# Kernel tuning notes

Measured on AMD Instinct MI355X. Metric: run time of the kernel, lower is better.

## Reference

```python
import jax, jax.numpy as jnp
import numpy as np

N_EVENTS = 16384
B = 4
H = W = 64
KH = KW = 3
P = KH * KW
D = 256  # input_size == hidden_size


def setup_inputs() -> dict:
    rng = np.random.default_rng(0)
    # events sorted by batch, time = arange (sorted within batch)
    batch_id = np.sort(rng.integers(0, B, N_EVENTS))
    hh = rng.integers(KH - 1, H - KH + 1, N_EVENTS)  # interior pixels -> exactly P patches each
    ww = rng.integers(KW - 1, W - KW + 1, N_EVENTS)
    time = np.arange(N_EVENTS)
    # scatter each event to its P=kh*kw overlapping patches (stride 1)
    Hp, Wp = H - KH + 1, W - KW + 1
    ki = np.arange(KH)[:, None]
    kj = np.arange(KW)[None, :]
    pos = (ki * KW + kj).reshape(1, P)                       # [1, P]
    pl = hh[:, None] - ki.reshape(1, -1).repeat(KW, 1).reshape(1, P) if False else None
    ki_f = np.repeat(np.arange(KH), KW)                       # [P]
    kj_f = np.tile(np.arange(KW), KH)                         # [P]
    patch_row = hh[:, None] - ki_f[None, :]                   # [N, P]
    patch_col = ww[:, None] - kj_f[None, :]
    patch_lin = (batch_id[:, None] * (Hp * Wp) + patch_row * Wp + patch_col).reshape(-1)
    pos_flat = np.broadcast_to((ki_f * KW + kj_f)[None, :], (N_EVENTS, P)).reshape(-1)
    orig_flat = np.repeat(np.arange(N_EVENTS), P)
    t_flat = np.repeat(time, P)
    order = np.lexsort((t_flat, patch_lin))                   # group by patch, time-ordered within
    patch_sorted = patch_lin[order]
    orig_event_idx = orig_flat[order].astype(np.int32)
    pos_id = pos_flat[order].astype(np.int32)
    seg_start = np.concatenate([[True], patch_sorted[1:] != patch_sorted[:-1]])

    key = jax.random.key(0)
    ks = jax.random.split(key, 8)
    std = np.sqrt(2.0 / (D + D)).astype(np.float32)
    lin = 1.0 / np.sqrt(D).astype(np.float32)
    return {
        "events": jax.random.normal(ks[0], (N_EVENTS, D), jnp.float32),
        "scatter_w": jax.random.normal(ks[1], (P, D, D), jnp.float32) * std,
        "gather_w": jax.random.normal(ks[2], (P, D, D), jnp.float32) * std,
        "q_w": jax.random.normal(ks[3], (D, D), jnp.float32) * lin,
        "v_w": jax.random.normal(ks[4], (D, D), jnp.float32) * lin,
        "g_w": jax.random.normal(ks[5], (D, D), jnp.float32) * lin,
        "o_w": jax.random.normal(ks[6], (D, D), jnp.float32) * lin,
        "ln_gamma": jnp.ones((D,), jnp.float32),
        "ln_beta": jnp.zeros((D,), jnp.float32),
        "orig_event_idx": jnp.asarray(orig_event_idx),
        "pos_id": jnp.asarray(pos_id),
        "seg_start": jnp.asarray(seg_start),
    }


def _pos_proj(x, weights, pos_id):
    # per-patch-position linear: out[n] = weights[pos_id[n]] @ x[n]
    # disjoint masks partition rows, so masked GEMMs sum exactly (mirrors torch loop)
    out = jnp.zeros((x.shape[0], weights.shape[1]), x.dtype)
    for i in range(weights.shape[0]):
        m = (pos_id == i)[:, None]
        out = out + jnp.where(m, x @ weights[i].T, 0.0)
    return out


def _gated_scan(g, v, seg_start):
    # h_t = g_t * h_{t-1} + (1 - g_t) * v_t, reset at segment starts
    a = jnp.where(seg_start[:, None], 0.0, g)
    b = (1.0 - g) * v
    def comb(c1, c2):
        a1, b1 = c1
        a2, b2 = c2
        return (a1 * a2, a2 * b1 + b2)
    _, h = jax.lax.associative_scan(comb, (a, b), axis=0)
    return h


def reference(events, scatter_w, gather_w, q_w, v_w, g_w, o_w, ln_gamma, ln_beta,
              orig_event_idx, pos_id, seg_start):
    x = events[orig_event_idx]                     # [M, D] scatter events -> patch copies
    y = _pos_proj(x, scatter_w, pos_id)            # indexed conv-like projection
    q = y @ q_w.T
    v = y @ v_w.T
    g = jax.nn.sigmoid(y @ g_w.T)
    h = _gated_scan(g, v, seg_start)               # ragged gated linear scan
    o = (q * h) @ o_w.T
    z = _pos_proj(o, gather_w, pos_id)             # indexed gather projection
    out = jnp.zeros_like(events).at[orig_event_idx].add(z)  # gather back (sum over P copies)
    out = out + events                             # residual (input_size == hidden_size)
    mu = jnp.mean(out, axis=-1, keepdims=True)
    var = jnp.mean(jnp.square(out - mu), axis=-1, keepdims=True)
    out = (out - mu) * jax.lax.rsqrt(var + 1e-5) * ln_gamma + ln_beta
    return out
```

## Files before the change

### kernel.cpp

```cpp
#include <hip/hip_runtime.h>

typedef __bf16 bf16x8 __attribute__((ext_vector_type(8)));
typedef float f32x4 __attribute__((ext_vector_type(4)));

#define NEV 16384
#define MTOT 147456
#define LDQ 2304
#define LDX 6912

__device__ __forceinline__ unsigned short f2bf(float f) {
  unsigned x = __float_as_uint(f);
  x += 0x7FFFu + ((x >> 16) & 1u);
  return (unsigned short)(x >> 16);
}
__device__ __forceinline__ float bf2f(unsigned short u) {
  return __uint_as_float(((unsigned)u) << 16);
}
__device__ __forceinline__ void load_lds16(const void* g, void* l) {
  __builtin_amdgcn_global_load_lds(
      (const __attribute__((address_space(1))) unsigned int*)g,
      (__attribute__((address_space(3))) unsigned int*)l, 16, 0, 0);
}

__global__ void k_cast4(const float* __restrict__ in, unsigned short* __restrict__ out, int n4) {
  int i = blockIdx.x * blockDim.x + threadIdx.x;
  if (i >= n4) return;
  float4 v = reinterpret_cast<const float4*>(in)[i];
  ushort4 o;
  o.x = f2bf(v.x); o.y = f2bf(v.y); o.z = f2bf(v.z); o.w = f2bf(v.w);
  reinterpret_cast<ushort4*>(out)[i] = o;
}

__global__ void k_cast3(const float* __restrict__ q, const float* __restrict__ v,
                        const float* __restrict__ g, unsigned short* __restrict__ out) {
  int which = blockIdx.y;
  const float* src = (which == 0) ? q : (which == 1) ? v : g;
  int i = blockIdx.x * blockDim.x + threadIdx.x;
  if (i >= 16384) return;
  float4 val = reinterpret_cast<const float4*>(src)[i];
  ushort4 o;
  o.x = f2bf(val.x); o.y = f2bf(val.y); o.z = f2bf(val.z); o.w = f2bf(val.w);
  reinterpret_cast<ushort4*>(out + (long)which * 65536)[i] = o;
}

__global__ __launch_bounds__(256) void k_transpose_t(const float* __restrict__ in,
                                                     unsigned short* __restrict__ out) {
  __shared__ float s[32][33];
  const int b = blockIdx.z;
  const int r0 = blockIdx.x * 32, c0 = blockIdx.y * 32;
  const int tx = threadIdx.x & 31, ty = threadIdx.x >> 5;
  const float* src = in + (long)b * 65536;
  unsigned short* dst = out + (long)b * 65536;
#pragma unroll
  for (int cc = 0; cc < 4; ++cc)
    s[ty + cc * 8][tx] = src[(c0 + ty + cc * 8) * 256 + r0 + tx];
  __syncthreads();
#pragma unroll
  for (int cc = 0; cc < 4; ++cc)
    dst[(long)(r0 + ty + cc * 8) * 256 + c0 + tx] = f2bf(s[tx][ty + cc * 8]);
}

__global__ void k_detect(const unsigned int* __restrict__ seg, int* mode) {
  __shared__ int fFloat, fGt1;
  if (threadIdx.x == 0) { fFloat = 0; fGt1 = 0; }
  __syncthreads();
  int lf = 0, lg = 0;
  for (int i = threadIdx.x; i < 1024; i += 256) {
    unsigned v = seg[i];
    if (v == 0x3F800000u) lf = 1;
    else if (v > 1u) lg = 1;
  }
  if (lf) atomicOr(&fFloat, 1);
  if (lg) atomicOr(&fGt1, 1);
  __syncthreads();
  if (threadIdx.x == 0) *mode = fFloat ? 2 : (fGt1 ? 1 : 0);
}

__device__ __forceinline__ bool is_start(const void* seg, int mode, int i) {
  if (mode == 1) return ((const unsigned char*)seg)[i] != 0;
  if (mode == 2) return ((const float*)seg)[i] != 0.0f;
  return ((const int*)seg)[i] != 0;
}

__global__ __launch_bounds__(256) void k_count(const void* __restrict__ seg,
                                               const int* __restrict__ modep,
                                               int* __restrict__ blockCounts) {
  __shared__ int wc[4];
  const int md = *modep;
  const int i = blockIdx.x * 256 + threadIdx.x;
  const bool f = is_start(seg, md, i);
  unsigned long long m = __ballot(f);
  const int lane = threadIdx.x & 63, wid = threadIdx.x >> 6;
  if (lane == 0) wc[wid] = __popcll(m);
  __syncthreads();
  if (threadIdx.x == 0) blockCounts[blockIdx.x] = wc[0] + wc[1] + wc[2] + wc[3];
}

__global__ __launch_bounds__(256) void k_emit(const void* __restrict__ seg,
                                              const int* __restrict__ modep,
                                              const int* __restrict__ blockCounts,
                                              int* __restrict__ starts, int* __restrict__ nsegp) {
  __shared__ int sh[12];
  const int md = *modep;
  const int bid = blockIdx.x, tid = threadIdx.x;
  const int lane = tid & 63, wid = tid >> 6;
  int part = 0;
  for (int j = tid; j < bid; j += 256) part += blockCounts[j];
  for (int o = 32; o; o >>= 1) part += __shfl_xor(part, o, 64);
  if (lane == 0) sh[wid] = part;
  if (bid == 0) {
    int tot = 0;
    for (int j = tid; j < 576; j += 256) tot += blockCounts[j];
    for (int o = 32; o; o >>= 1) tot += __shfl_xor(tot, o, 64);
    if (lane == 0) sh[8 + wid] = tot;
  }
  const int i = bid * 256 + tid;
  const bool f = is_start(seg, md, i);
  unsigned long long m = __ballot(f);
  if (lane == 0) sh[4 + wid] = __popcll(m);
  __syncthreads();
  const int base = sh[0] + sh[1] + sh[2] + sh[3];
  int wpre = 0;
#pragma unroll
  for (int w2 = 0; w2 < 4; ++w2) if (w2 < wid) wpre += sh[4 + w2];
  if (bid == 0 && tid == 0) *nsegp = sh[8] + sh[9] + sh[10] + sh[11];
  if (f) {
    const int lanePre = __popcll(m & ((1ull << lane) - 1));
    starts[base + wpre + lanePre] = i;
  }
}

template<bool F32OUT>
__device__ __forceinline__ void gemm_tile(
    const unsigned short* __restrict__ A, const unsigned short* __restrict__ B,
    void* __restrict__ Cv, int r0, int c0, int K, int lda, int ldb, int ldc,
    unsigned short* As, unsigned short* Bs) {
  const int tid = threadIdx.x, lane = tid & 63, wid = tid >> 6;
  const int wr = (wid >> 1) * 64, wc = (wid & 1) * 64;
  const int la = lane & 15, lb2 = lane >> 4;
  const int arow = tid >> 2;
  const int cs = ((tid & 3) ^ ((arow >> 1) & 3)) * 8;
  const int nk = K >> 5;
  f32x4 acc[4][4];
#pragma unroll
  for (int i = 0; i < 4; ++i)
#pragma unroll
    for (int j = 0; j < 4; ++j) acc[i][j] = (f32x4)0.0f;

  const unsigned short* ga0 = A + (long)(r0 + arow) * lda + cs;
  const unsigned short* gb0 = B + (long)(c0 + arow) * ldb + cs;

  load_lds16(ga0, &As[tid * 8]);
  load_lds16(ga0 + (long)64 * lda, &As[2048 + tid * 8]);
  load_lds16(gb0, &Bs[tid * 8]);
  load_lds16(gb0 + (long)64 * ldb, &Bs[2048 + tid * 8]);
  __syncthreads();

  for (int k = 0; k < nk; ++k) {
    if (k + 1 < nk) {
      const int nb = ((k + 1) & 1) * 4096;
      const unsigned short* ga = ga0 + (k + 1) * 32;
      const unsigned short* gb = gb0 + (k + 1) * 32;
      load_lds16(ga, &As[nb + tid * 8]);
      load_lds16(ga + (long)64 * lda, &As[nb + 2048 + tid * 8]);
      load_lds16(gb, &Bs[nb + tid * 8]);
      load_lds16(gb + (long)64 * ldb, &Bs[nb + 2048 + tid * 8]);
    }
    const int cb = (k & 1) * 4096;
    bf16x8 af[4], bv[4];
#pragma unroll
    for (int i = 0; i < 4; ++i) {
      const int ra = wr + i * 16 + la;
      const int rb = wc + i * 16 + la;
      af[i] = *reinterpret_cast<const bf16x8*>(&As[cb + ra * 32 + ((lb2 ^ ((ra >> 1) & 3)) * 8)]);
      bv[i] = *reinterpret_cast<const bf16x8*>(&Bs[cb + rb * 32 + ((lb2 ^ ((rb >> 1) & 3)) * 8)]);
    }
#pragma unroll
    for (int i = 0; i < 4; ++i)
#pragma unroll
      for (int j = 0; j < 4; ++j)
        acc[i][j] = __builtin_amdgcn_mfma_f32_16x16x32_bf16(af[i], bv[j], acc[i][j], 0, 0, 0);
    __syncthreads();
  }
#pragma unroll
  for (int i = 0; i < 4; ++i)
#pragma unroll
    for (int j = 0; j < 4; ++j)
#pragma unroll
      for (int r = 0; r < 4; ++r) {
        const int row = r0 + wr + i * 16 + lb2 * 4 + r;
        const int col = c0 + wc + j * 16 + la;
        if (F32OUT) ((float*)Cv)[(long)row * ldc + col] = acc[i][j][r];
        else ((unsigned short*)Cv)[(long)row * ldc + col] = f2bf(acc[i][j][r]);
      }
}

__global__ __launch_bounds__(256) void k_wgemm(
    const unsigned short* __restrict__ qvgw, const unsigned short* __restrict__ wt,
    const unsigned short* __restrict__ gaw, const unsigned short* __restrict__ owt,
    unsigned short* __restrict__ ABig, unsigned short* __restrict__ Bo2) {
  __shared__ __align__(16) unsigned short As[8192];
  __shared__ __align__(16) unsigned short Bs[8192];
  const int b = blockIdx.z;
  const unsigned short *A, *B;
  unsigned short* C;
  int ldc;
  if (b < 27) {
    A = qvgw + (long)(b / 9) * 65536;
    B = wt + (long)(b % 9) * 65536;
    C = ABig + (long)b * 65536; ldc = 256;
  } else {
    A = gaw + (long)(b - 27) * 65536;
    B = owt;
    C = Bo2 + (b - 27) * 256; ldc = LDQ;
  }
  gemm_tile<false>(A, B, C, blockIdx.x * 128, blockIdx.y * 128, 256, 256, 256, ldc, As, Bs);
}

__global__ __launch_bounds__(256) void k_qvg3(
    const unsigned short* __restrict__ ev, const unsigned short* __restrict__ ABig,
    unsigned short* __restrict__ X) {
  __shared__ __align__(16) unsigned short As[8192];
  __shared__ __align__(16) unsigned short Bs[3][4096];
  const int p = blockIdx.z;
  const int r0 = blockIdx.x * 128, c0 = blockIdx.y * 64;
  const int tid = threadIdx.x, lane = tid & 63, wid = tid >> 6;
  const int wr2 = (wid >> 1) * 64, wc2 = (wid & 1) * 32;
  const int la = lane & 15, lb2 = lane >> 4;
  f32x4 acc[3][4][2];
#pragma unroll
  for (int w = 0; w < 3; ++w)
#pragma unroll
    for (int i = 0; i < 4; ++i)
#pragma unroll
      for (int j = 0; j < 2; ++j) acc[w][i][j] = (f32x4)0.0f;

  for (int k0 = 0; k0 < 256; k0 += 64) {
#pragma unroll
    for (int q = 0; q < 4; ++q) {
      const int g = q * 256 + tid;
      const int row = g >> 3, c = g & 7;
      load_lds16(ev + (long)(r0 + row) * 256 + k0 + ((c ^ (row & 7)) * 8), &As[g * 8]);
    }
#pragma unroll
    for (int w = 0; w < 3; ++w) {
      const unsigned short* Bw = ABig + (long)(w * 9 + p) * 65536;
#pragma unroll
      for (int q = 0; q < 2; ++q) {
        const int g = q * 256 + tid;
        const int row = g >> 3, c = g & 7;
        load_lds16(Bw + (long)(c0 + row) * 256 + k0 + ((c ^ (row & 7)) * 8), &Bs[w][g * 8]);
      }
    }
    __syncthreads();
#pragma unroll
    for (int kk = 0; kk < 2; ++kk) {
      bf16x8 af[4], bv[3][2];
#pragma unroll
      for (int i = 0; i < 4; ++i) {
        const int ra = wr2 + i * 16 + la;
        const int slot = (kk * 4 + lb2) ^ (ra & 7);
        af[i] = *reinterpret_cast<const bf16x8*>(&As[ra * 64 + slot * 8]);
      }
#pragma unroll
      for (int w = 0; w < 3; ++w)
#pragma unroll
        for (int j = 0; j < 2; ++j) {
          const int rb = wc2 + j * 16 + la;
          const int slot = (kk * 4 + lb2) ^ (rb & 7);
          bv[w][j] = *reinterpret_cast<const bf16x8*>(&Bs[w][rb * 64 + slot * 8]);
        }
#pragma unroll
      for (int w = 0; w < 3; ++w)
#pragma unroll
        for (int i = 0; i < 4; ++i)
#pragma unroll
          for (int j = 0; j < 2; ++j)
            acc[w][i][j] = __builtin_amdgcn_mfma_f32_16x16x32_bf16(af[i], bv[w][j], acc[w][i][j], 0, 0, 0);
    }
    __syncthreads();
  }
#pragma unroll
  for (int w = 0; w < 3; ++w) {
    unsigned short* Xw = X + p * 768 + w * 256;
#pragma unroll
    for (int i = 0; i < 4; ++i)
#pragma unroll
      for (int j = 0; j < 2; ++j)
#pragma unroll
        for (int r = 0; r < 4; ++r) {
          const int row = r0 + wr2 + i * 16 + lb2 * 4 + r;
          const int col = c0 + wc2 + j * 16 + la;
          Xw[(long)row * LDX + col] = f2bf(acc[w][i][j][r]);
        }
  }
}

__global__ __launch_bounds__(256) void k_scan(
    unsigned short* __restrict__ X,
    const int* __restrict__ starts, const int* __restrict__ cntp, const int* __restrict__ modep,
    const void* __restrict__ seg, const int* __restrict__ pos_id, const int* __restrict__ oidx) {
  const int lane = threadIdx.x & 63;
  const int w = blockIdx.x * 4 + (threadIdx.x >> 6);
  const int nW = gridDim.x * 4;
  const int nseg = *cntp;
  const int md = *modep;
  for (int s = w; s < nseg; s += nW) {
    int t = starts[s];
    int p = pos_id[t], e = oidx[t];
    long base = (long)e * LDX + p * 768 + lane * 4;
    ushort4 ql = *(const ushort4*)(X + base);
    ushort4 vl = *(const ushort4*)(X + base + 256);
    ushort4 gl = *(const ushort4*)(X + base + 512);
    bool cont = (t + 1 < MTOT) && !is_start(seg, md, t + 1);
    float h0 = 0.f, h1 = 0.f, h2 = 0.f, h3 = 0.f;
    for (;;) {
      ushort4 qn, vn, gn;
      long nbase = 0;
      bool cont2 = false;
      if (cont) {
        int pn = pos_id[t + 1], en = oidx[t + 1];
        nbase = (long)en * LDX + pn * 768 + lane * 4;
        qn = *(const ushort4*)(X + nbase);
        vn = *(const ushort4*)(X + nbase + 256);
        gn = *(const ushort4*)(X + nbase + 512);
        cont2 = (t + 2 < MTOT) && !is_start(seg, md, t + 2);
      }
      float g0 = 1.f / (1.f + __expf(-bf2f(gl.x)));
      float g1 = 1.f / (1.f + __expf(-bf2f(gl.y)));
      float g2 = 1.f / (1.f + __expf(-bf2f(gl.z)));
      float g3 = 1.f / (1.f + __expf(-bf2f(gl.w)));
      h0 = g0 * h0 + (1.f - g0) * bf2f(vl.x);
      h1 = g1 * h1 + (1.f - g1) * bf2f(vl.y);
      h2 = g2 * h2 + (1.f - g2) * bf2f(vl.z);
      h3 = g3 * h3 + (1.f - g3) * bf2f(vl.w);
      ushort4 o;
      o.x = f2bf(bf2f(ql.x) * h0);
      o.y = f2bf(bf2f(ql.y) * h1);
      o.z = f2bf(bf2f(ql.z) * h2);
      o.w = f2bf(bf2f(ql.w) * h3);
      *(ushort4*)(X + base + 256) = o;
      if (!cont) break;
      ++t;
      base = nbase; ql = qn; vl = vn; gl = gn; cont = cont2;
    }
  }
}

__global__ __launch_bounds__(256) void k_p5(
    const unsigned short* __restrict__ X, const unsigned short* __restrict__ Bo2,
    const float* __restrict__ ev, float* __restrict__ S) {
  __shared__ __align__(16) unsigned short As[4096];
  __shared__ __align__(16) unsigned short Bs[4096];
  const int r0 = blockIdx.x * 128, c0 = blockIdx.y * 128;
  const int tid = threadIdx.x, lane = tid & 63, wid = tid >> 6;
  const int wr = (wid >> 1) * 64, wc = (wid & 1) * 64;
  const int la = lane & 15, lb2 = lane >> 4;
  const int arow = tid >> 2;
  const int cs = ((tid & 3) ^ ((arow >> 1) & 3)) * 8;
  f32x4 acc[4][4];
#pragma unroll
  for (int i = 0; i < 4; ++i)
#pragma unroll
    for (int j = 0; j < 4; ++j) acc[i][j] = (f32x4)0.0f;

  for (int kc = 0; kc < 72; ++kc) {
    const int p = kc >> 3, nn = (kc & 7) * 32;
    const unsigned short* ga = X + (long)(r0 + arow) * LDX + p * 768 + 256 + nn + cs;
    const unsigned short* gb = Bo2 + (long)(c0 + arow) * LDQ + p * 256 + nn + cs;
    load_lds16(ga, &As[tid * 8]);
    load_lds16(ga + (long)64 * LDX, &As[2048 + tid * 8]);
    load_lds16(gb, &Bs[tid * 8]);
    load_lds16(gb + (long)64 * LDQ, &Bs[2048 + tid * 8]);
    __syncthreads();
    bf16x8 af[4], bv[4];
#pragma unroll
    for (int i = 0; i < 4; ++i) {
      const int ra = wr + i * 16 + la;
      const int rb = wc + i * 16 + la;
      af[i] = *reinterpret_cast<const bf16x8*>(&As[ra * 32 + ((lb2 ^ ((ra >> 1) & 3)) * 8)]);
      bv[i] = *reinterpret_cast<const bf16x8*>(&Bs[rb * 32 + ((lb2 ^ ((rb >> 1) & 3)) * 8)]);
    }
#pragma unroll
    for (int i = 0; i < 4; ++i)
#pragma unroll
      for (int j = 0; j < 4; ++j)
        acc[i][j] = __builtin_amdgcn_mfma_f32_16x16x32_bf16(af[i], bv[j], acc[i][j], 0, 0, 0);
    __syncthreads();
  }
#pragma unroll
  for (int i = 0; i < 4; ++i)
#pragma unroll
    for (int j = 0; j < 4; ++j)
#pragma unroll
      for (int r = 0; r < 4; ++r) {
        const int row = r0 + wr + i * 16 + lb2 * 4 + r;
        const int col = c0 + wc + j * 16 + la;
        S[(long)row * 256 + col] = acc[i][j][r] + ev[(long)row * 256 + col];
      }
}

__global__ __launch_bounds__(256) void k_ln(float* __restrict__ S,
                                            const float* __restrict__ gamma, const float* __restrict__ beta) {
  int row = blockIdx.x * 4 + (threadIdx.x >> 6);
  int lane = threadIdx.x & 63;
  long base = (long)row * 256 + lane * 4;
  float4 s4 = *reinterpret_cast<const float4*>(S + base);
  float v0 = s4.x, v1 = s4.y, v2 = s4.z, v3 = s4.w;
  float s = v0 + v1 + v2 + v3;
  float ss = v0 * v0 + v1 * v1 + v2 * v2 + v3 * v3;
  for (int o = 32; o; o >>= 1) { s += __shfl_xor(s, o, 64); ss += __shfl_xor(ss, o, 64); }
  float mu = s * (1.0f / 256.0f);
  float var = ss * (1.0f / 256.0f) - mu * mu;
  float rs = rsqrtf(fmaxf(var, 0.0f) + 1e-5f);
  float4 g4 = *reinterpret_cast<const float4*>(gamma + lane * 4);
  float4 b4 = *reinterpret_cast<const float4*>(beta + lane * 4);
  float4 o4;
  o4.x = (v0 - mu) * rs * g4.x + b4.x;
  o4.y = (v1 - mu) * rs * g4.y + b4.y;
  o4.z = (v2 - mu) * rs * g4.z + b4.z;
  o4.w = (v3 - mu) * rs * g4.w + b4.w;
  *reinterpret_cast<float4*>(S + base) = o4;
}

extern "C" void kernel_launch(void* const* d_in, const int* in_sizes, int n_in,
                              void* d_out, int out_size, void* d_ws, size_t ws_size,
                              hipStream_t stream) {
  const float* events    = (const float*)d_in[0];
  const float* scatter_w = (const float*)d_in[1];
  const float* gather_w  = (const float*)d_in[2];
  const float* q_w       = (const float*)d_in[3];
  const float* v_w       = (const float*)d_in[4];
  const float* g_w       = (const float*)d_in[5];
  const float* o_w       = (const float*)d_in[6];
  const float* ln_gamma  = (const float*)d_in[7];
  const float* ln_beta   = (const float*)d_in[8];
  const int*   oidx      = (const int*)d_in[9];
  const int*   pos_id    = (const int*)d_in[10];
  const void*  seg       = d_in[11];
  float* out = (float*)d_out;

  char* base = (char*)d_ws;
  int* counter = (int*)base;
  int* mode    = (int*)(base + 4);
  int* blockCounts = (int*)(base + 64);
  int* starts  = (int*)(base + 4096);
  unsigned short* ev_bf  = (unsigned short*)(base + 598016);
  unsigned short* wt     = (unsigned short*)(base + 8986624);
  unsigned short* qvgw   = (unsigned short*)(base + 10166272);
  unsigned short* owt    = (unsigned short*)(base + 10559488);
  unsigned short* gaw_bf = (unsigned short*)(base + 10690560);
  unsigned short* ABig   = (unsigned short*)(base + 11870208);
  unsigned short* Bo2    = (unsigned short*)(base + 15409152);
  unsigned short* X      = (unsigned short*)(base + 16588800);

  k_detect<<<1, 256, 0, stream>>>((const unsigned int*)seg, mode);

  k_cast4<<<4096, 256, 0, stream>>>(events, ev_bf, 1048576);
  k_cast3<<<dim3(64, 3), 256, 0, stream>>>(q_w, v_w, g_w, qvgw);
  k_cast4<<<576, 256, 0, stream>>>(gather_w, gaw_bf, 147456);
  k_transpose_t<<<dim3(8, 8, 9), 256, 0, stream>>>(scatter_w, wt);
  k_transpose_t<<<dim3(8, 8, 1), 256, 0, stream>>>(o_w, owt);

  k_wgemm<<<dim3(2, 2, 36), 256, 0, stream>>>(qvgw, wt, gaw_bf, owt, ABig, Bo2);

  k_qvg3<<<dim3(128, 4, 9), 256, 0, stream>>>(ev_bf, ABig, X);

  k_count<<<576, 256, 0, stream>>>(seg, mode, blockCounts);
  k_emit<<<576, 256, 0, stream>>>(seg, mode, blockCounts, starts, counter);
  k_scan<<<2048, 256, 0, stream>>>(X, starts, counter, mode, seg, pos_id, oidx);

  k_p5<<<dim3(128, 2), 256, 0, stream>>>(X, Bo2, events, out);
  k_ln<<<4096, 256, 0, stream>>>(out, ln_gamma, ln_beta);
}
```

Measured before the change: 228.3 us.

## Fuse cast kernels, merge transposes, and fold LayerNorm into final GEMM

```diff
diff --git a/kernel.cpp b/kernel.cpp
--- a/kernel.cpp
+++ b/kernel.cpp
@@ -22,35 +22,40 @@
       (__attribute__((address_space(3))) unsigned int*)l, 16, 0, 0);
 }
 
-__global__ void k_cast4(const float* __restrict__ in, unsigned short* __restrict__ out, int n4) {
+__global__ void k_prep(const float* __restrict__ events, const float* __restrict__ q,
+                       const float* __restrict__ v, const float* __restrict__ g,
+                       const float* __restrict__ gaw,
+                       unsigned short* __restrict__ ev_bf, unsigned short* __restrict__ qvgw,
+                       unsigned short* __restrict__ gaw_bf) {
   int i = blockIdx.x * blockDim.x + threadIdx.x;
-  if (i >= n4) return;
-  float4 v = reinterpret_cast<const float4*>(in)[i];
-  ushort4 o;
-  o.x = f2bf(v.x); o.y = f2bf(v.y); o.z = f2bf(v.z); o.w = f2bf(v.w);
-  reinterpret_cast<ushort4*>(out)[i] = o;
-}
-
-__global__ void k_cast3(const float* __restrict__ q, const float* __restrict__ v,
-                        const float* __restrict__ g, unsigned short* __restrict__ out) {
-  int which = blockIdx.y;
-  const float* src = (which == 0) ? q : (which == 1) ? v : g;
-  int i = blockIdx.x * blockDim.x + threadIdx.x;
-  if (i >= 16384) return;
-  float4 val = reinterpret_cast<const float4*>(src)[i];
+  const float* src;
+  unsigned short* dst;
+  int off;
+  if (i < 1048576) { src = events; dst = ev_bf; off = i; }
+  else if (i < 1097728) {
+    int j = i - 1048576;
+    int w = j >> 14;
+    src = (w == 0) ? q : (w == 1) ? v : g;
+    dst = qvgw + (long)w * 65536;
+    off = j & 16383;
+  } else if (i < 1245184) { src = gaw; dst = gaw_bf; off = i - 1097728; }
+  else return;
+  float4 val = reinterpret_cast<const float4*>(src)[off];
   ushort4 o;
   o.x = f2bf(val.x); o.y = f2bf(val.y); o.z = f2bf(val.z); o.w = f2bf(val.w);
-  reinterpret_cast<ushort4*>(out + (long)which * 65536)[i] = o;
-}
-
-__global__ __launch_bounds__(256) void k_transpose_t(const float* __restrict__ in,
-                                                     unsigned short* __restrict__ out) {
+  reinterpret_cast<ushort4*>(dst)[off] = o;
+}
+
+__global__ __launch_bounds__(256) void k_transpose_t(const float* __restrict__ sw,
+                                                     const float* __restrict__ ow,
+                                                     unsigned short* __restrict__ wt,
+                                                     unsigned short* __restrict__ owt) {
   __shared__ float s[32][33];
-  const int b = blockIdx.z;
+  const int z = blockIdx.z;
+  const float* src = (z < 9) ? sw + (long)z * 65536 : ow;
+  unsigned short* dst = (z < 9) ? wt + (long)z * 65536 : owt;
   const int r0 = blockIdx.x * 32, c0 = blockIdx.y * 32;
   const int tx = threadIdx.x & 31, ty = threadIdx.x >> 5;
-  const float* src = in + (long)b * 65536;
-  unsigned short* dst = out + (long)b * 65536;
 #pragma unroll
   for (int cc = 0; cc < 4; ++cc)
     s[ty + cc * 8][tx] = src[(c0 + ty + cc * 8) * 256 + r0 + tx];
@@ -130,10 +135,9 @@
   }
 }
 
-template<bool F32OUT>
 __device__ __forceinline__ void gemm_tile(
     const unsigned short* __restrict__ A, const unsigned short* __restrict__ B,
-    void* __restrict__ Cv, int r0, int c0, int K, int lda, int ldb, int ldc,
+    unsigned short* __restrict__ C, int r0, int c0, int K, int lda, int ldb, int ldc,
     unsigned short* As, unsigned short* Bs) {
   const int tid = threadIdx.x, lane = tid & 63, wid = tid >> 6;
   const int wr = (wid >> 1) * 64, wc = (wid & 1) * 64;
@@ -190,8 +194,7 @@
       for (int r = 0; r < 4; ++r) {
         const int row = r0 + wr + i * 16 + lb2 * 4 + r;
         const int col = c0 + wc + j * 16 + la;
-        if (F32OUT) ((float*)Cv)[(long)row * ldc + col] = acc[i][j][r];
-        else ((unsigned short*)Cv)[(long)row * ldc + col] = f2bf(acc[i][j][r]);
+        C[(long)row * ldc + col] = f2bf(acc[i][j][r]);
       }
 }
 
@@ -214,7 +217,7 @@
     B = owt;
     C = Bo2 + (b - 27) * 256; ldc = LDQ;
   }
-  gemm_tile<false>(A, B, C, blockIdx.x * 128, blockIdx.y * 128, 256, 256, 256, ldc, As, Bs);
+  gemm_tile(A, B, C, blockIdx.x * 128, blockIdx.y * 128, 256, 256, 256, ldc, As, Bs);
 }
 
 __global__ __launch_bounds__(256) void k_qvg3(
@@ -347,17 +350,21 @@
   }
 }
 
-__global__ __launch_bounds__(256) void k_p5(
+__global__ __launch_bounds__(512) void k_p5ln(
     const unsigned short* __restrict__ X, const unsigned short* __restrict__ Bo2,
-    const float* __restrict__ ev, float* __restrict__ S) {
+    const float* __restrict__ ev, const float* __restrict__ gamma,
+    const float* __restrict__ beta, float* __restrict__ out) {
   __shared__ __align__(16) unsigned short As[4096];
-  __shared__ __align__(16) unsigned short Bs[4096];
-  const int r0 = blockIdx.x * 128, c0 = blockIdx.y * 128;
+  __shared__ __align__(16) unsigned short Bs[8192];
+  __shared__ float rsum[128], rsumsq[128];
+  const int r0 = blockIdx.x * 128;
   const int tid = threadIdx.x, lane = tid & 63, wid = tid >> 6;
-  const int wr = (wid >> 1) * 64, wc = (wid & 1) * 64;
+  const int wr = (wid >> 2) * 64, wc = (wid & 3) * 64;
   const int la = lane & 15, lb2 = lane >> 4;
-  const int arow = tid >> 2;
-  const int cs = ((tid & 3) ^ ((arow >> 1) & 3)) * 8;
+  if (tid < 128) { rsum[tid] = 0.0f; rsumsq[tid] = 0.0f; }
+
+  const int arowA = tid >> 2;
+  const int csA = ((tid & 3) ^ ((arowA >> 1) & 3)) * 8;
   f32x4 acc[4][4];
 #pragma unroll
   for (int i = 0; i < 4; ++i)
@@ -366,12 +373,14 @@
 
   for (int kc = 0; kc < 72; ++kc) {
     const int p = kc >> 3, nn = (kc & 7) * 32;
-    const unsigned short* ga = X + (long)(r0 + arow) * LDX + p * 768 + 256 + nn + cs;
-    const unsigned short* gb = Bo2 + (long)(c0 + arow) * LDQ + p * 256 + nn + cs;
-    load_lds16(ga, &As[tid * 8]);
-    load_lds16(ga + (long)64 * LDX, &As[2048 + tid * 8]);
-    load_lds16(gb, &Bs[tid * 8]);
-    load_lds16(gb + (long)64 * LDQ, &Bs[2048 + tid * 8]);
+    load_lds16(X + (long)(r0 + arowA) * LDX + p * 768 + 256 + nn + csA, &As[tid * 8]);
+#pragma unroll
+    for (int q = 0; q < 2; ++q) {
+      const int g = q * 512 + tid;
+      const int rowB = g >> 2;
+      const int cB = ((g & 3) ^ ((rowB >> 1) & 3)) * 8;
+      load_lds16(Bo2 + (long)rowB * LDQ + p * 256 + nn + cB, &Bs[g * 8]);
+    }
     __syncthreads();
     bf16x8 af[4], bv[4];
 #pragma unroll
@@ -388,39 +397,40 @@
         acc[i][j] = __builtin_amdgcn_mfma_f32_16x16x32_bf16(af[i], bv[j], acc[i][j], 0, 0, 0);
     __syncthreads();
   }
+
 #pragma unroll
   for (int i = 0; i < 4; ++i)
 #pragma unroll
-    for (int j = 0; j < 4; ++j)
-#pragma unroll
-      for (int r = 0; r < 4; ++r) {
-        const int row = r0 + wr + i * 16 + lb2 * 4 + r;
-        const int col = c0 + wc + j * 16 + la;
-        S[(long)row * 256 + col] = acc[i][j][r] + ev[(long)row * 256 + col];
-      }
-}
-
-__global__ __launch_bounds__(256) void k_ln(float* __restrict__ S,
-                                            const float* __restrict__ gamma, const float* __restrict__ beta) {
-  int row = blockIdx.x * 4 + (threadIdx.x >> 6);
-  int lane = threadIdx.x & 63;
-  long base = (long)row * 256 + lane * 4;
-  float4 s4 = *reinterpret_cast<const float4*>(S + base);
-  float v0 = s4.x, v1 = s4.y, v2 = s4.z, v3 = s4.w;
-  float s = v0 + v1 + v2 + v3;
-  float ss = v0 * v0 + v1 * v1 + v2 * v2 + v3 * v3;
-  for (int o = 32; o; o >>= 1) { s += __shfl_xor(s, o, 64); ss += __shfl_xor(ss, o, 64); }
-  float mu = s * (1.0f / 256.0f);
-  float var = ss * (1.0f / 256.0f) - mu * mu;
-  float rs = rsqrtf(fmaxf(var, 0.0f) + 1e-5f);
-  float4 g4 = *reinterpret_cast<const float4*>(gamma + lane * 4);
-  float4 b4 = *reinterpret_cast<const float4*>(beta + lane * 4);
-  float4 o4;
-  o4.x = (v0 - mu) * rs * g4.x + b4.x;
-  o4.y = (v1 - mu) * rs * g4.y + b4.y;
-  o4.z = (v2 - mu) * rs * g4.z + b4.z;
-  o4.w = (v3 - mu) * rs * g4.w + b4.w;
-  *reinterpret_cast<float4*>(S + base) = o4;
+    for (int r = 0; r < 4; ++r) {
+      const int row = wr + i * 16 + lb2 * 4 + r;
+      float ps = 0.0f, pss = 0.0f;
+#pragma unroll
+      for (int j = 0; j < 4; ++j) {
+        const int col = wc + j * 16 + la;
+        float v = acc[i][j][r] + ev[(long)(r0 + row) * 256 + col];
+        acc[i][j][r] = v;
+        ps += v; pss += v * v;
+      }
+#pragma unroll
+      for (int o = 8; o; o >>= 1) { ps += __shfl_xor(ps, o, 64); pss += __shfl_xor(pss, o, 64); }
+      if (la == 0) { atomicAdd(&rsum[row], ps); atomicAdd(&rsumsq[row], pss); }
+    }
+  __syncthreads();
+#pragma unroll
+  for (int i = 0; i < 4; ++i)
+#pragma unroll
+    for (int r = 0; r < 4; ++r) {
+      const int row = wr + i * 16 + lb2 * 4 + r;
+      const float mu = rsum[row] * (1.0f / 256.0f);
+      const float var = rsumsq[row] * (1.0f / 256.0f) - mu * mu;
+      const float rs = rsqrtf(fmaxf(var, 0.0f) + 1e-5f);
+#pragma unroll
+      for (int j = 0; j < 4; ++j) {
+        const int col = wc + j * 16 + la;
+        out[(long)(r0 + row) * 256 + col] =
+            (acc[i][j][r] - mu) * rs * gamma[col] + beta[col];
+      }
+    }
 }
 
 extern "C" void kernel_launch(void* const* d_in, const int* in_sizes, int n_in,
@@ -456,11 +466,8 @@
 
   k_detect<<<1, 256, 0, stream>>>((const unsigned int*)seg, mode);
 
-  k_cast4<<<4096, 256, 0, stream>>>(events, ev_bf, 1048576);
-  k_cast3<<<dim3(64, 3), 256, 0, stream>>>(q_w, v_w, g_w, qvgw);
-  k_cast4<<<576, 256, 0, stream>>>(gather_w, gaw_bf, 147456);
-  k_transpose_t<<<dim3(8, 8, 9), 256, 0, stream>>>(scatter_w, wt);
-  k_transpose_t<<<dim3(8, 8, 1), 256, 0, stream>>>(o_w, owt);
+  k_prep<<<4864, 256, 0, stream>>>(events, q_w, v_w, g_w, gather_w, ev_bf, qvgw, gaw_bf);
+  k_transpose_t<<<dim3(8, 8, 10), 256, 0, stream>>>(scatter_w, o_w, wt, owt);
 
   k_wgemm<<<dim3(2, 2, 36), 256, 0, stream>>>(qvgw, wt, gaw_bf, owt, ABig, Bo2);
 
@@ -470,6 +477,5 @@
   k_emit<<<576, 256, 0, stream>>>(seg, mode, blockCounts, starts, counter);
   k_scan<<<2048, 256, 0, stream>>>(X, starts, counter, mode, seg, pos_id, oidx);
 
-  k_p5<<<dim3(128, 2), 256, 0, stream>>>(X, Bo2, events, out);
-  k_ln<<<4096, 256, 0, stream>>>(out, ln_gamma, ln_beta);
-}
+  k_p5ln<<<128, 512, 0, stream>>>(X, Bo2, events, ln_gamma, ln_beta, out);
+}
```

Result: slower. 236.2 us (+3.5%).

## Merge cast/transpose launches and widen qvg3 tile to 128 columns with 512 threads

Applied to the files above, without the earlier changes.

```diff
diff --git a/kernel.cpp b/kernel.cpp
--- a/kernel.cpp
+++ b/kernel.cpp
@@ -22,35 +22,40 @@
       (__attribute__((address_space(3))) unsigned int*)l, 16, 0, 0);
 }
 
-__global__ void k_cast4(const float* __restrict__ in, unsigned short* __restrict__ out, int n4) {
+__global__ void k_prep(const float* __restrict__ events, const float* __restrict__ q,
+                       const float* __restrict__ v, const float* __restrict__ g,
+                       const float* __restrict__ gaw,
+                       unsigned short* __restrict__ ev_bf, unsigned short* __restrict__ qvgw,
+                       unsigned short* __restrict__ gaw_bf) {
   int i = blockIdx.x * blockDim.x + threadIdx.x;
-  if (i >= n4) return;
-  float4 v = reinterpret_cast<const float4*>(in)[i];
-  ushort4 o;
-  o.x = f2bf(v.x); o.y = f2bf(v.y); o.z = f2bf(v.z); o.w = f2bf(v.w);
-  reinterpret_cast<ushort4*>(out)[i] = o;
-}
-
-__global__ void k_cast3(const float* __restrict__ q, const float* __restrict__ v,
-                        const float* __restrict__ g, unsigned short* __restrict__ out) {
-  int which = blockIdx.y;
-  const float* src = (which == 0) ? q : (which == 1) ? v : g;
-  int i = blockIdx.x * blockDim.x + threadIdx.x;
-  if (i >= 16384) return;
-  float4 val = reinterpret_cast<const float4*>(src)[i];
+  const float* src;
+  unsigned short* dst;
+  int off;
+  if (i < 1048576) { src = events; dst = ev_bf; off = i; }
+  else if (i < 1097728) {
+    int j = i - 1048576;
+    int w = j >> 14;
+    src = (w == 0) ? q : (w == 1) ? v : g;
+    dst = qvgw + (long)w * 65536;
+    off = j & 16383;
+  } else if (i < 1245184) { src = gaw; dst = gaw_bf; off = i - 1097728; }
+  else return;
+  float4 val = reinterpret_cast<const float4*>(src)[off];
   ushort4 o;
   o.x = f2bf(val.x); o.y = f2bf(val.y); o.z = f2bf(val.z); o.w = f2bf(val.w);
-  reinterpret_cast<ushort4*>(out + (long)which * 65536)[i] = o;
-}
-
-__global__ __launch_bounds__(256) void k_transpose_t(const float* __restrict__ in,
-                                                     unsigned short* __restrict__ out) {
+  reinterpret_cast<ushort4*>(dst)[off] = o;
+}
+
+__global__ __launch_bounds__(256) void k_transpose_t(const float* __restrict__ sw,
+                                                     const float* __restrict__ ow,
+                                                     unsigned short* __restrict__ wt,
+                                                     unsigned short* __restrict__ owt) {
   __shared__ float s[32][33];
-  const int b = blockIdx.z;
+  const int z = blockIdx.z;
+  const float* src = (z < 9) ? sw + (long)z * 65536 : ow;
+  unsigned short* dst = (z < 9) ? wt + (long)z * 65536 : owt;
   const int r0 = blockIdx.x * 32, c0 = blockIdx.y * 32;
   const int tx = threadIdx.x & 31, ty = threadIdx.x >> 5;
-  const float* src = in + (long)b * 65536;
-  unsigned short* dst = out + (long)b * 65536;
 #pragma unroll
   for (int cc = 0; cc < 4; ++cc)
     s[ty + cc * 8][tx] = src[(c0 + ty + cc * 8) * 256 + r0 + tx];
@@ -130,10 +135,9 @@
   }
 }
 
-template<bool F32OUT>
 __device__ __forceinline__ void gemm_tile(
     const unsigned short* __restrict__ A, const unsigned short* __restrict__ B,
-    void* __restrict__ Cv, int r0, int c0, int K, int lda, int ldb, int ldc,
+    unsigned short* __restrict__ C, int r0, int c0, int K, int lda, int ldb, int ldc,
     unsigned short* As, unsigned short* Bs) {
   const int tid = threadIdx.x, lane = tid & 63, wid = tid >> 6;
   const int wr = (wid >> 1) * 64, wc = (wid & 1) * 64;
@@ -190,8 +194,7 @@
       for (int r = 0; r < 4; ++r) {
         const int row = r0 + wr + i * 16 + lb2 * 4 + r;
         const int col = c0 + wc + j * 16 + la;
-        if (F32OUT) ((float*)Cv)[(long)row * ldc + col] = acc[i][j][r];
-        else ((unsigned short*)Cv)[(long)row * ldc + col] = f2bf(acc[i][j][r]);
+        C[(long)row * ldc + col] = f2bf(acc[i][j][r]);
       }
 }
 
@@ -214,18 +217,18 @@
     B = owt;
     C = Bo2 + (b - 27) * 256; ldc = LDQ;
   }
-  gemm_tile<false>(A, B, C, blockIdx.x * 128, blockIdx.y * 128, 256, 256, 256, ldc, As, Bs);
-}
-
-__global__ __launch_bounds__(256) void k_qvg3(
+  gemm_tile(A, B, C, blockIdx.x * 128, blockIdx.y * 128, 256, 256, 256, ldc, As, Bs);
+}
+
+__global__ __launch_bounds__(512) void k_qvg3(
     const unsigned short* __restrict__ ev, const unsigned short* __restrict__ ABig,
     unsigned short* __restrict__ X) {
   __shared__ __align__(16) unsigned short As[8192];
-  __shared__ __align__(16) unsigned short Bs[3][4096];
+  __shared__ __align__(16) unsigned short Bs[3][8192];
   const int p = blockIdx.z;
-  const int r0 = blockIdx.x * 128, c0 = blockIdx.y * 64;
+  const int r0 = blockIdx.x * 128, c0 = blockIdx.y * 128;
   const int tid = threadIdx.x, lane = tid & 63, wid = tid >> 6;
-  const int wr2 = (wid >> 1) * 64, wc2 = (wid & 1) * 32;
+  const int wr2 = (wid >> 2) * 64, wc2 = (wid & 3) * 32;
   const int la = lane & 15, lb2 = lane >> 4;
   f32x4 acc[3][4][2];
 #pragma unroll
@@ -237,8 +240,8 @@
 
   for (int k0 = 0; k0 < 256; k0 += 64) {
 #pragma unroll
-    for (int q = 0; q < 4; ++q) {
-      const int g = q * 256 + tid;
+    for (int q = 0; q < 2; ++q) {
+      const int g = q * 512 + tid;
       const int row = g >> 3, c = g & 7;
       load_lds16(ev + (long)(r0 + row) * 256 + k0 + ((c ^ (row & 7)) * 8), &As[g * 8]);
     }
@@ -247,7 +250,7 @@
       const unsigned short* Bw = ABig + (long)(w * 9 + p) * 65536;
 #pragma unroll
       for (int q = 0; q < 2; ++q) {
-        const int g = q * 256 + tid;
+        const int g = q * 512 + tid;
         const int row = g >> 3, c = g & 7;
         load_lds16(Bw + (long)(c0 + row) * 256 + k0 + ((c ^ (row & 7)) * 8), &Bs[w][g * 8]);
       }
@@ -456,15 +459,12 @@
 
   k_detect<<<1, 256, 0, stream>>>((const unsigned int*)seg, mode);
 
-  k_cast4<<<4096, 256, 0, stream>>>(events, ev_bf, 1048576);
-  k_cast3<<<dim3(64, 3), 256, 0, stream>>>(q_w, v_w, g_w, qvgw);
-  k_cast4<<<576, 256, 0, stream>>>(gather_w, gaw_bf, 147456);
-  k_transpose_t<<<dim3(8, 8, 9), 256, 0, stream>>>(scatter_w, wt);
-  k_transpose_t<<<dim3(8, 8, 1), 256, 0, stream>>>(o_w, owt);
+  k_prep<<<4864, 256, 0, stream>>>(events, q_w, v_w, g_w, gather_w, ev_bf, qvgw, gaw_bf);
+  k_transpose_t<<<dim3(8, 8, 10), 256, 0, stream>>>(scatter_w, o_w, wt, owt);
 
   k_wgemm<<<dim3(2, 2, 36), 256, 0, stream>>>(qvgw, wt, gaw_bf, owt, ABig, Bo2);
 
-  k_qvg3<<<dim3(128, 4, 9), 256, 0, stream>>>(ev_bf, ABig, X);
+  k_qvg3<<<dim3(128, 2, 9), 512, 0, stream>>>(ev_bf, ABig, X);
 
   k_count<<<576, 256, 0, stream>>>(seg, mode, blockCounts);
   k_emit<<<576, 256, 0, stream>>>(seg, mode, blockCounts, starts, counter);
```

Result: slower. 244.6 us (+7.1%).
